# Kernel tuning notes

Hardware: AMD Instinct MI355X
Metric: run time of the kernel (lower is better)

## Reference

```python
import jax, jax.numpy as jnp
import numpy as np

HIDDEN = 2048
N_HEADS = 16
N_KV = 8
HEAD_DIM = 128
EPS = 1e-6
THETA = 1000000.0
T = 2048


def _rmsnorm(x, w):
    # x: [T, h, D]; normalize over last dim
    var = jnp.mean(x * x, axis=-1, keepdims=True)
    return x * jax.lax.rsqrt(var + EPS) * w


def _rope(x, positions):
    # neox-style rotate-half, rotary_dim == head_dim
    D = x.shape[-1]
    inv_freq = 1.0 / (THETA ** (jnp.arange(0, D, 2, dtype=jnp.float32) / D))  # [D/2]
    freqs = positions.astype(jnp.float32)[:, None] * inv_freq  # [T, D/2]
    cos = jnp.cos(freqs)[:, None, :]  # [T, 1, D/2]
    sin = jnp.sin(freqs)[:, None, :]
    x1, x2 = jnp.split(x, 2, axis=-1)
    return jnp.concatenate([x1 * cos - x2 * sin, x2 * cos + x1 * sin], axis=-1)


def setup_inputs() -> dict:
    key = jax.random.key(0)
    ks = jax.random.split(key, 7)
    s = 0.02
    return {
        "positions": jnp.arange(T, dtype=jnp.int32),
        "hidden_states": jax.random.normal(ks[0], (T, HIDDEN), dtype=jnp.float32),
        "wq": jax.random.normal(ks[1], (HIDDEN, N_HEADS * HEAD_DIM), dtype=jnp.float32) * s,
        "wk": jax.random.normal(ks[2], (HIDDEN, N_KV * HEAD_DIM), dtype=jnp.float32) * s,
        "wv": jax.random.normal(ks[3], (HIDDEN, N_KV * HEAD_DIM), dtype=jnp.float32) * s,
        "wo": jax.random.normal(ks[4], (N_HEADS * HEAD_DIM, HIDDEN), dtype=jnp.float32) * s,
        "q_norm_w": jnp.ones((HEAD_DIM,), dtype=jnp.float32),
        "k_norm_w": jnp.ones((HEAD_DIM,), dtype=jnp.float32),
    }


def reference(positions, hidden_states, wq, wk, wv, wo, q_norm_w, k_norm_w):
    q = (hidden_states @ wq).reshape(-1, N_HEADS, HEAD_DIM)
    k = (hidden_states @ wk).reshape(-1, N_KV, HEAD_DIM)
    v = (hidden_states @ wv).reshape(-1, N_KV, HEAD_DIM)
    q = _rmsnorm(q, q_norm_w)
    k = _rmsnorm(k, k_norm_w)
    q = _rope(q, positions)
    k = _rope(k, positions)
    # GQA: expand kv heads
    rep = N_HEADS // N_KV
    k = jnp.repeat(k, rep, axis=1)  # [T, H, D]
    v = jnp.repeat(v, rep, axis=1)
    scale = HEAD_DIM ** -0.5
    scores = jnp.einsum('qhd,khd->hqk', q, k) * scale  # [H, T, T]
    tq = q.shape[0]
    causal = jnp.tril(jnp.ones((tq, tq), dtype=bool))
    scores = jnp.where(causal[None], scores, jnp.finfo(scores.dtype).min)
    probs = jax.nn.softmax(scores, axis=-1)
    o = jnp.einsum('hqk,khd->qhd', probs, v).reshape(tq, N_HEADS * HEAD_DIM)
    return o @ wo
```

## Files before the change

### kernel.cpp

```cpp
#include <hip/hip_runtime.h>
#include <cstdint>

#define TT 2048
#define NH 16
#define NKV 8
#define HD 128
#define SCALE_L2E 0.12751743f
#define SM_M2 16.5f

typedef unsigned short u16;
typedef unsigned int u32;
typedef u16 u16x8 __attribute__((ext_vector_type(8)));
typedef u32 u32x2 __attribute__((ext_vector_type(2)));
typedef __bf16 bf16x8 __attribute__((ext_vector_type(8)));
typedef float f32x4 __attribute__((ext_vector_type(4)));
typedef float f32x16 __attribute__((ext_vector_type(16)));

__device__ inline u16 f2bf(float x){
  u32 u = __builtin_bit_cast(u32, x);
  u = (u + 0x7fffu + ((u >> 16) & 1u)) >> 16;
  return (u16)u;
}
__device__ inline float bf2f(u16 h){
  return __builtin_bit_cast(float, (u32)h << 16);
}
__device__ inline bf16x8 as_bf(u16x8 v){ return __builtin_bit_cast(bf16x8, v); }

__device__ inline void gl_lds16(const void* g, void* l){
  typedef __attribute__((address_space(1))) const void gv_t;
  typedef __attribute__((address_space(3))) void lv_t;
  __builtin_amdgcn_global_load_lds((gv_t*)g, (lv_t*)l, 16, 0, 0);
}

__global__ void cast_f32_bf16(const float* __restrict__ in, u16* __restrict__ out, int n8){
  int i = blockIdx.x * blockDim.x + threadIdx.x;
  if (i < n8){
    const float4* p = (const float4*)(in + (size_t)i * 8);
    float4 a = p[0], b = p[1];
    u16x8 o = { f2bf(a.x), f2bf(a.y), f2bf(a.z), f2bf(a.w),
                f2bf(b.x), f2bf(b.y), f2bf(b.z), f2bf(b.w) };
    *(u16x8*)(out + (size_t)i * 8) = o;
  }
}

__global__ void transpose_cast(const float* __restrict__ in, u16* __restrict__ out, int R, int C){
  __shared__ float tile[64][65];
  int bx = blockIdx.x * 64;
  int by = blockIdx.y * 64;
  int tid = threadIdx.x;
  #pragma unroll
  for (int i = 0; i < 4; ++i){
    int idx = i * 256 + tid;
    int r = idx >> 4, c4 = (idx & 15) * 4;
    float4 v = *(const float4*)&in[(size_t)(by + r) * C + bx + c4];
    tile[r][c4] = v.x; tile[r][c4 + 1] = v.y; tile[r][c4 + 2] = v.z; tile[r][c4 + 3] = v.w;
  }
  __syncthreads();
  #pragma unroll
  for (int i = 0; i < 2; ++i){
    int idx = i * 256 + tid;
    int cc = idx >> 3, s8 = (idx & 7) * 8;
    u16x8 o;
    #pragma unroll
    for (int j = 0; j < 8; ++j) o[j] = f2bf(tile[s8 + j][cc]);
    *(u16x8*)&out[(size_t)(bx + cc) * R + by + s8] = o;
  }
}

template<bool F32OUT>
__global__ __launch_bounds__(512, 2) void gemm8p(const u16* __restrict__ A, const u16* __restrict__ B,
                                                 void* __restrict__ Cv, int Klen,
                                                 int lda, int ldb, int ldc, size_t zstride){
  extern __shared__ u16 smem[];
  const int tid = threadIdx.x;
  const int wv = tid >> 6, ln = tid & 63;
  const int lg = ln >> 4, l15 = ln & 15;
  const int wr = wv >> 2, wc = wv & 3;
  const int nbx = gridDim.x;
  const int orig = blockIdx.x + nbx * blockIdx.y;
  const int cpx = (nbx * gridDim.y) >> 3;
  const int swz = (orig & 7) * cpx + (orig >> 3);
  const int m0 = (swz / nbx) * 128, n0 = (swz % nbx) * 256;
  const int Kofs = blockIdx.z * Klen;
  const u16* Ab0 = A + (size_t)m0 * lda + Kofs;
  const u16* Bb0 = B + (size_t)n0 * ldb + Kofs;
  f32x4 acc[4][4] = {};

  auto stage = [&](int sbuf, int kt, int part){
    u16* base = smem + sbuf * 24576;
    if (part == 0){
      const u16* Ak = Ab0 + kt * 64;
      #pragma unroll
      for (int it = 0; it < 2; ++it){
        int idx = it * 512 + tid;
        int r = idx >> 3, sl = idx & 7, g = sl ^ (r & 7);
        gl_lds16(Ak + (size_t)r * lda + g * 8, base + (it * 512 + wv * 64) * 8);
      }
      const u16* Bk = Bb0 + kt * 64;
      { int idx = tid; int r = idx >> 3, sl = idx & 7, g = sl ^ (r & 7);
        gl_lds16(Bk + (size_t)r * ldb + g * 8, base + (8192 + wv * 64 * 8)); }
    } else {
      const u16* Bk = Bb0 + kt * 64;
      #pragma unroll
      for (int it = 1; it < 4; ++it){
        int idx = it * 512 + tid;
        int r = idx >> 3, sl = idx & 7, g = sl ^ (r & 7);
        gl_lds16(Bk + (size_t)r * ldb + g * 8, base + (8192 + (it * 512 + wv * 64) * 8));
      }
    }
  };

  bf16x8 a0[4], b0[4], a1[4], b1[4];
  auto ldfrags = [&](const u16* lA, bf16x8* af, bf16x8* bf, int kk){
    const u16* lB = lA + 8192;
    #pragma unroll
    for (int mm = 0; mm < 4; mm++){
      int ra = wr * 64 + mm * 16 + l15;
      int sl = (kk * 4 + lg) ^ (ra & 7);
      af[mm] = as_bf(*(const u16x8*)&lA[(ra * 8 + sl) * 8]);
    }
    #pragma unroll
    for (int nn = 0; nn < 4; nn++){
      int cb = wc * 64 + nn * 16 + l15;
      int sl = (kk * 4 + lg) ^ (cb & 7);
      bf[nn] = as_bf(*(const u16x8*)&lB[(cb * 8 + sl) * 8]);
    }
  };
  auto mfma16 = [&](bf16x8* af, bf16x8* bf){
    __builtin_amdgcn_s_setprio(1);
    #pragma unroll
    for (int mm = 0; mm < 4; mm++)
      #pragma unroll
      for (int nn = 0; nn < 4; nn++)
        acc[mm][nn] = __builtin_amdgcn_mfma_f32_16x16x32_bf16(af[mm], bf[nn], acc[mm][nn], 0, 0, 0);
    __builtin_amdgcn_s_setprio(0);
  };

  const int nk = Klen / 64;
  stage(0, 0, 0); stage(0, 0, 1);
  stage(1, 1, 0); stage(1, 1, 1);
  asm volatile("s_waitcnt vmcnt(6)" ::: "memory");
  asm volatile("s_barrier" ::: "memory");
  ldfrags(smem, a0, b0, 0);

  for (int kt = 0; kt < nk; ++kt){
    const u16* lA = smem + (kt % 3) * 24576;
    ldfrags(lA, a1, b1, 1);
    if (kt + 2 < nk) stage((kt + 2) % 3, kt + 2, 0);
    mfma16(a0, b0);
    if (kt + 2 < nk)      asm volatile("s_waitcnt vmcnt(3)" ::: "memory");
    else if (kt + 1 < nk) asm volatile("s_waitcnt vmcnt(0)" ::: "memory");
    asm volatile("s_barrier" ::: "memory");
    if (kt + 1 < nk)
      ldfrags(smem + ((kt + 1) % 3) * 24576, a0, b0, 0);
    if (kt + 2 < nk) stage((kt + 2) % 3, kt + 2, 1);
    mfma16(a1, b1);
    asm volatile("s_barrier" ::: "memory");
  }
  #pragma unroll
  for (int mm = 0; mm < 4; mm++)
    #pragma unroll
    for (int nn = 0; nn < 4; nn++){
      int grow0 = m0 + wr * 64 + mm * 16 + lg * 4;
      int gcol  = n0 + wc * 64 + nn * 16 + l15;
      #pragma unroll
      for (int r = 0; r < 4; r++){
        float v = acc[mm][nn][r];
        if (F32OUT) ((float*)Cv + blockIdx.z * zstride)[(size_t)(grow0 + r) * ldc + gcol] = v;
        else        ((u16*)Cv)[(size_t)(grow0 + r) * ldc + gcol] = f2bf(v);
      }
    }
}

__global__ void add_f32(const float* __restrict__ a, const float* __restrict__ b,
                        float* __restrict__ o, int n4){
  int i = blockIdx.x * blockDim.x + threadIdx.x;
  if (i < n4){
    float4 x = ((const float4*)a)[i], y = ((const float4*)b)[i];
    float4 z = { x.x + y.x, x.y + y.y, x.z + y.z, x.w + y.w };
    ((float4*)o)[i] = z;
  }
}

__global__ void rmsnorm_rope(const u16* __restrict__ QKV, const int* __restrict__ pos,
                             const float* __restrict__ qw, const float* __restrict__ kw,
                             u16* __restrict__ Qr, u16* __restrict__ Kr){
  int gw = (blockIdx.x * blockDim.x + threadIdx.x) >> 6;
  int ln = threadIdx.x & 63;
  int t = gw / 24, idx = gw % 24;
  if (t >= TT) return;
  bool isq = idx < NH;
  int head = isq ? idx : idx - NH;
  const u16* src = QKV + (size_t)t * 4096 + (isq ? head * HD : 2048 + head * HD);
  const float* wgt = isq ? qw : kw;
  float x0 = bf2f(src[ln]), x1 = bf2f(src[ln + 64]);
  float ss = x0 * x0 + x1 * x1;
  #pragma unroll
  for (int off = 32; off; off >>= 1) ss += __shfl_xor(ss, off);
  float r = rsqrtf(ss * (1.0f / 128.0f) + 1e-6f);
  float xn0 = x0 * r * wgt[ln], xn1 = x1 * r * wgt[ln + 64];
  float inv = exp2f(-(float)ln * 0.311430758895690f);
  float ang = (float)pos[t] * inv;
  float c = cosf(ang), s = sinf(ang);
  float o0 = xn0 * c - xn1 * s;
  float o1 = xn1 * c + xn0 * s;
  u16* dst = isq ? (Qr + (size_t)t * 2048 + head * HD) : (Kr + (size_t)t * 1024 + head * HD);
  dst[ln]      = f2bf(o0);
  dst[ln + 64] = f2bf(o1);
}

__global__ void v_transpose(const u16* __restrict__ QKV, u16* __restrict__ Vt){
  __shared__ u16 tile[64][72];
  int kh = blockIdx.z;
  int d0 = blockIdx.y * 64;
  int t0 = blockIdx.x * 64;
  int tid = threadIdx.x;
  #pragma unroll
  for (int it = 0; it < 2; ++it){
    int idx = it * 256 + tid;
    int tr = idx >> 3, seg = idx & 7;
    *(u16x8*)&tile[tr][seg * 8] =
      *(const u16x8*)(QKV + (size_t)(t0 + tr) * 4096 + 3072 + kh * HD + d0 + seg * 8);
  }
  __syncthreads();
  #pragma unroll
  for (int it = 0; it < 2; ++it){
    int idx = it * 256 + tid;
    int dr = idx >> 3, seg = idx & 7;
    u16x8 v;
    #pragma unroll
    for (int j = 0; j < 8; j++) v[j] = tile[seg * 8 + j][dr];
    *(u16x8*)(Vt + ((size_t)kh * HD + d0 + dr) * 2048 + t0 + seg * 8) = v;
  }
}

__global__ __launch_bounds__(512, 4) void attn(const u16* __restrict__ Qr, const u16* __restrict__ Kr,
                                               const u16* __restrict__ Vt, u16* __restrict__ O){
  extern __shared__ u16 smem[];
  u16* Karea = smem;
  u16* Varea = smem + 16384;
  u16* Parea = smem + 32768;
  const int h = blockIdx.y, kh = h >> 1;
  const int qc = (h < 8) ? blockIdx.x : 31 - blockIdx.x;
  const int tid = threadIdx.x, wv = tid >> 6, ln = tid & 63;
  const bool isS = wv < 4;
  const int role = wv & 3;
  const int qw = role & 1, jp = role >> 1;
  const int q5 = ln & 31, hb = ln >> 5;
  const int nit = qc + 1;

  auto stage = [&](int i){
    if (i + 1 < nit){
      u16* Kd = Karea + ((i + 1) & 1) * 8192;
      #pragma unroll
      for (int j = 0; j < 2; ++j){
        int lin = j * 512 + tid;
        int tok = lin >> 4, seg = lin & 15;
        gl_lds16(Kr + (size_t)((i + 1) * 64 + tok) * 1024 + kh * HD + (seg ^ (tok & 7)) * 8,
                 Kd + (j * 512 + wv * 64) * 8);
      }
    }
    if (i < nit){
      u16* Vd = Varea + (i & 1) * 8192;
      #pragma unroll
      for (int j = 0; j < 2; ++j){
        int lin = j * 512 + tid;
        int d = lin >> 3, sl = lin & 7;
        gl_lds16(Vt + (size_t)kh * HD * 2048 + (size_t)d * 2048 + i * 64 + (sl ^ (d & 7)) * 8,
                 Vd + (j * 512 + wv * 64) * 8);
      }
    }
  };

  #pragma unroll
  for (int j = 0; j < 2; ++j){
    int lin = j * 512 + tid;
    int tok = lin >> 4, seg = lin & 15;
    gl_lds16(Kr + (size_t)tok * 1024 + kh * HD + (seg ^ (tok & 7)) * 8,
             Karea + (j * 512 + wv * 64) * 8);
  }

  const u16x8 ones_u = {0x3f80, 0x3f80, 0x3f80, 0x3f80, 0x3f80, 0x3f80, 0x3f80, 0x3f80};
  const bf16x8 onesf = as_bf(ones_u);

  if (isS){
    bf16x8 qf[8];
    {
      const u16* qp = Qr + (size_t)(qc * 64 + qw * 32 + q5) * 2048 + h * HD + hb * 8;
      #pragma unroll
      for (int s = 0; s < 8; ++s) qf[s] = as_bf(*(const u16x8*)(qp + s * 16));
    }
    u16* Pq = Parea + role * 1280 + q5 * 40;
    for (int i = 0; i <= nit; ++i){
      __syncthreads();
      stage(i);
      const int t = 2 * i + jp;
      const int D0 = 32 * t - 64 * qc - 32 * qw;
      const bool act = (i < nit) && (D0 <= 0);
      f32x16 c = {};
      if (act){
        const u16* Kb = Karea + (i & 1) * 8192;
        const int tokIdx = 32 * jp + q5;
        __builtin_amdgcn_s_setprio(1);
        #pragma unroll
        for (int s = 0; s < 8; ++s){
          int seg = (2 * s + hb) ^ (q5 & 7);
          bf16x8 kf = as_bf(*(const u16x8*)&Kb[tokIdx * 128 + seg * 8]);
          c = __builtin_amdgcn_mfma_f32_32x32x16_bf16(kf, qf[s], c, 0, 0, 0);
        }
        __builtin_amdgcn_s_setprio(0);
      }
      asm volatile("s_barrier" ::: "memory");
      if (act){
        const bool diag = (D0 == 0);
        u32 pk[8];
        #pragma unroll
        for (int j = 0; j < 8; ++j){
          float pv[2];
          #pragma unroll
          for (int e = 0; e < 2; ++e){
            int r = 2 * j + e;
            int tok = (r & 3) + 8 * (r >> 2) + 4 * hb;
            float x = c[r] * SCALE_L2E - SM_M2;
            if (diag && tok > q5) x = -1e30f;
            pv[e] = exp2f(x);
          }
          pk[j] = (__builtin_bit_cast(u32, pv[0]) >> 16) |
                  (__builtin_bit_cast(u32, pv[1]) & 0xffff0000u);
        }
        *(u32x2*)&Pq[hb * 4 +  0] = u32x2{pk[0], pk[1]};
        *(u32x2*)&Pq[hb * 4 +  8] = u32x2{pk[2], pk[3]};
        *(u32x2*)&Pq[hb * 4 + 16] = u32x2{pk[4], pk[5]};
        *(u32x2*)&Pq[hb * 4 + 24] = u32x2{pk[6], pk[7]};
      }
    }
    __syncthreads();
    __syncthreads();
  } else {
    f32x16 acc[4] = {};
    f32x16 asum = {};
    const u16* Pw = Parea + role * 1280;
    for (int i = 0; i <= nit; ++i){
      __syncthreads();
      stage(i);
      const int t = 2 * (i - 1) + jp;
      const int D0 = 32 * t - 64 * qc - 32 * qw;
      const bool act = (i >= 1) && (D0 <= 0);
      bf16x8 pf0 = {}, pf1 = {};
      if (act){
        pf0 = as_bf(*(const u16x8*)&Pw[q5 * 40 + hb * 8]);
        pf1 = as_bf(*(const u16x8*)&Pw[q5 * 40 + 16 + hb * 8]);
        asm volatile("s_waitcnt lgkmcnt(0)" ::: "memory");
        __builtin_amdgcn_sched_barrier(0);
      }
      asm volatile("s_barrier" ::: "memory");
      if (act){
        const u16* Vb = Varea + ((i - 1) & 1) * 8192;
        __builtin_amdgcn_s_setprio(1);
        #pragma unroll
        for (int s2 = 0; s2 < 2; ++s2){
          bf16x8 pf = s2 ? pf1 : pf0;
          asum = __builtin_amdgcn_mfma_f32_32x32x16_bf16(pf, onesf, asum, 0, 0, 0);
          #pragma unroll
          for (int dblk = 0; dblk < 4; ++dblk){
            int d = dblk * 32 + q5;
            int sl = (4 * jp + 2 * s2 + hb) ^ (d & 7);
            bf16x8 vf = as_bf(*(const u16x8*)&Vb[d * 64 + sl * 8]);
            acc[dblk] = __builtin_amdgcn_mfma_f32_32x32x16_bf16(pf, vf, acc[dblk], 0, 0, 0);
          }
        }
        __builtin_amdgcn_s_setprio(0);
      }
    }
    __syncthreads();
    float* Ls  = (float*)smem;
    float* LsS = (float*)smem + 8192;
    if (jp == 1){
      #pragma unroll
      for (int dblk = 0; dblk < 4; ++dblk)
        #pragma unroll
        for (int r = 0; r < 16; ++r){
          int qrow = (r & 3) + 8 * (r >> 2) + 4 * hb;
          Ls[qw * 4096 + qrow * 128 + dblk * 32 + q5] = acc[dblk][r];
        }
      if (q5 == 0){
        #pragma unroll
        for (int r = 0; r < 16; ++r){
          int qrow = (r & 3) + 8 * (r >> 2) + 4 * hb;
          LsS[qw * 32 + qrow] = asum[r];
        }
      }
    }
    __syncthreads();
    if (jp == 0){
      #pragma unroll
      for (int r = 0; r < 16; ++r){
        int qrow = (r & 3) + 8 * (r >> 2) + 4 * hb;
        float rs = 1.0f / (asum[r] + LsS[qw * 32 + qrow]);
        int qg = qc * 64 + qw * 32 + qrow;
        #pragma unroll
        for (int dblk = 0; dblk < 4; ++dblk){
          float o = (acc[dblk][r] + Ls[qw * 4096 + qrow * 128 + dblk * 32 + q5]) * rs;
          O[(size_t)qg * 2048 + h * HD + dblk * 32 + q5] = f2bf(o);
        }
      }
    }
  }
}

extern "C" void kernel_launch(void* const* d_in, const int* in_sizes, int n_in,
                              void* d_out, int out_size, void* d_ws, size_t ws_size,
                              hipStream_t stream){
  const int*   positions = (const int*)d_in[0];
  const float* hidden    = (const float*)d_in[1];
  const float* wq        = (const float*)d_in[2];
  const float* wk        = (const float*)d_in[3];
  const float* wv        = (const float*)d_in[4];
  const float* wo        = (const float*)d_in[5];
  const float* qw        = (const float*)d_in[6];
  const float* kw        = (const float*)d_in[7];
  float* out = (float*)d_out;

  char* ws = (char*)d_ws;
  u16* hs   = (u16*)ws; ws += (size_t)2048 * 2048 * 2;
  u16* Wqkv = (u16*)ws; ws += (size_t)4096 * 2048 * 2;
  u16* Wo   = (u16*)ws; ws += (size_t)2048 * 2048 * 2;
  u16* QKV  = (u16*)ws; ws += (size_t)2048 * 4096 * 2;
  u16* Qr   = (u16*)ws; ws += (size_t)2048 * 2048 * 2;
  u16* Kr   = (u16*)ws; ws += (size_t)2048 * 1024 * 2;
  u16* Vt   = (u16*)ws; ws += (size_t)8 * 128 * 2048 * 2;
  u16* O    = (u16*)ws;

  cast_f32_bf16<<<2048, 256, 0, stream>>>(hidden, hs, 2048 * 2048 / 8);
  transpose_cast<<<dim3(32, 32), 256, 0, stream>>>(wq, Wqkv, 2048, 2048);
  transpose_cast<<<dim3(16, 32), 256, 0, stream>>>(wk, Wqkv + (size_t)2048 * 2048, 2048, 1024);
  transpose_cast<<<dim3(16, 32), 256, 0, stream>>>(wv, Wqkv + (size_t)3072 * 2048, 2048, 1024);
  transpose_cast<<<dim3(32, 32), 256, 0, stream>>>(wo, Wo, 2048, 2048);

  gemm8p<false><<<dim3(16, 16, 1), 512, 147456, stream>>>(hs, Wqkv, QKV, 2048, 2048, 2048, 4096, 0);

  rmsnorm_rope<<<2048 * 24 / 4, 256, 0, stream>>>(QKV, positions, qw, kw, Qr, Kr);
  v_transpose<<<dim3(32, 2, 8), 256, 0, stream>>>(QKV, Vt);

  attn<<<dim3(32, 16), 512, 75776, stream>>>(Qr, Kr, Vt, O);

  float* p0 = (float*)QKV;
  gemm8p<true><<<dim3(8, 16, 2), 512, 147456, stream>>>(O, Wo, p0, 1024, 2048, 2048, 2048,
                                                        (size_t)2048 * 2048);
  add_f32<<<4096, 256, 0, stream>>>(p0, p0 + (size_t)2048 * 2048, out, 2048 * 2048 / 4);
}
```

Baseline: 154.3 us.

## Balance causal attention work by pairing query chunks and splitting KV across blocks

Each attention block now handles a pair of query chunks (p and 31-p). The KV range is split between two blocks, so every block walks 16 or 17 key tiles instead of a count that varies with causal position. Partial outputs and row sums for the upper chunk go to fp32 scratch buffers, and a new attn_norm kernel adds and normalizes them. The PV waves now split the head dimension instead of the key dimension, which removes the in-block LDS reduction. This costs an extra kernel launch and fp32 partial traffic, and it reuses the hs/Wqkv workspace as scratch.

```diff
diff --git a/kernel.cpp b/kernel.cpp
--- a/kernel.cpp
+++ b/kernel.cpp
@@ -235,49 +235,60 @@
 }
 
 __global__ __launch_bounds__(512, 4) void attn(const u16* __restrict__ Qr, const u16* __restrict__ Kr,
-                                               const u16* __restrict__ Vt, u16* __restrict__ O){
+                                               const u16* __restrict__ Vt, u16* __restrict__ O,
+                                               float* __restrict__ PB0, float* __restrict__ PB1,
+                                               float* __restrict__ RS0, float* __restrict__ RS1){
   extern __shared__ u16 smem[];
   u16* Karea = smem;
   u16* Varea = smem + 16384;
   u16* Parea = smem + 32768;
+  const int p = blockIdx.x & 15, half = blockIdx.x >> 4;
   const int h = blockIdx.y, kh = h >> 1;
-  const int qc = (h < 8) ? blockIdx.x : 31 - blockIdx.x;
+  const int c1 = p, c2 = 31 - p;
+  const int nst = half ? 16 : 17;
   const int tid = threadIdx.x, wv = tid >> 6, ln = tid & 63;
   const bool isS = wv < 4;
   const int role = wv & 3;
   const int qw = role & 1, jp = role >> 1;
   const int q5 = ln & 31, hb = ln >> 5;
-  const int nit = qc + 1;
-
-  auto stage = [&](int i){
-    if (i + 1 < nit){
-      u16* Kd = Karea + ((i + 1) & 1) * 8192;
-      #pragma unroll
-      for (int j = 0; j < 2; ++j){
-        int lin = j * 512 + tid;
+
+  auto ktof = [&](int j)->int { return half ? (16 - p + j) : ((j <= p) ? j : j - p - 1); };
+  auto chof = [&](int j)->int { return (half == 0 && j <= p) ? c1 : c2; };
+
+  auto stage = [&](int j){
+    if (j + 1 < nst){
+      int kt = ktof(j + 1);
+      u16* Kd = Karea + ((j + 1) & 1) * 8192;
+      #pragma unroll
+      for (int jj = 0; jj < 2; ++jj){
+        int lin = jj * 512 + tid;
         int tok = lin >> 4, seg = lin & 15;
-        gl_lds16(Kr + (size_t)((i + 1) * 64 + tok) * 1024 + kh * HD + (seg ^ (tok & 7)) * 8,
-                 Kd + (j * 512 + wv * 64) * 8);
-      }
-    }
-    if (i < nit){
-      u16* Vd = Varea + (i & 1) * 8192;
-      #pragma unroll
-      for (int j = 0; j < 2; ++j){
-        int lin = j * 512 + tid;
+        gl_lds16(Kr + (size_t)(kt * 64 + tok) * 1024 + kh * HD + (seg ^ (tok & 7)) * 8,
+                 Kd + (jj * 512 + wv * 64) * 8);
+      }
+    }
+    if (j < nst){
+      int kt = ktof(j);
+      u16* Vd = Varea + (j & 1) * 8192;
+      #pragma unroll
+      for (int jj = 0; jj < 2; ++jj){
+        int lin = jj * 512 + tid;
         int d = lin >> 3, sl = lin & 7;
-        gl_lds16(Vt + (size_t)kh * HD * 2048 + (size_t)d * 2048 + i * 64 + (sl ^ (d & 7)) * 8,
-                 Vd + (j * 512 + wv * 64) * 8);
+        gl_lds16(Vt + (size_t)kh * HD * 2048 + (size_t)d * 2048 + kt * 64 + (sl ^ (d & 7)) * 8,
+                 Vd + (jj * 512 + wv * 64) * 8);
       }
     }
   };
 
-  #pragma unroll
-  for (int j = 0; j < 2; ++j){
-    int lin = j * 512 + tid;
-    int tok = lin >> 4, seg = lin & 15;
-    gl_lds16(Kr + (size_t)tok * 1024 + kh * HD + (seg ^ (tok & 7)) * 8,
-             Karea + (j * 512 + wv * 64) * 8);
+  {
+    int kt = ktof(0);
+    #pragma unroll
+    for (int jj = 0; jj < 2; ++jj){
+      int lin = jj * 512 + tid;
+      int tok = lin >> 4, seg = lin & 15;
+      gl_lds16(Kr + (size_t)(kt * 64 + tok) * 1024 + kh * HD + (seg ^ (tok & 7)) * 8,
+               Karea + (jj * 512 + wv * 64) * 8);
+    }
   }
 
   const u16x8 ones_u = {0x3f80, 0x3f80, 0x3f80, 0x3f80, 0x3f80, 0x3f80, 0x3f80, 0x3f80};
@@ -286,47 +297,55 @@
   if (isS){
     bf16x8 qf[8];
     {
-      const u16* qp = Qr + (size_t)(qc * 64 + qw * 32 + q5) * 2048 + h * HD + hb * 8;
+      int c0 = half ? c2 : c1;
+      const u16* qp = Qr + (size_t)(c0 * 64 + qw * 32 + q5) * 2048 + h * HD + hb * 8;
       #pragma unroll
       for (int s = 0; s < 8; ++s) qf[s] = as_bf(*(const u16x8*)(qp + s * 16));
     }
     u16* Pq = Parea + role * 1280 + q5 * 40;
-    for (int i = 0; i <= nit; ++i){
+    for (int j = 0; j <= nst; ++j){
       __syncthreads();
-      stage(i);
-      const int t = 2 * i + jp;
-      const int D0 = 32 * t - 64 * qc - 32 * qw;
-      const bool act = (i < nit) && (D0 <= 0);
+      stage(j);
+      if (half == 0 && j == p + 1){
+        const u16* qp = Qr + (size_t)(c2 * 64 + qw * 32 + q5) * 2048 + h * HD + hb * 8;
+        #pragma unroll
+        for (int s = 0; s < 8; ++s) qf[s] = as_bf(*(const u16x8*)(qp + s * 16));
+      }
+      bool act = false, diag = false;
       f32x16 c = {};
-      if (act){
-        const u16* Kb = Karea + (i & 1) * 8192;
-        const int tokIdx = 32 * jp + q5;
-        __builtin_amdgcn_s_setprio(1);
-        #pragma unroll
-        for (int s = 0; s < 8; ++s){
-          int seg = (2 * s + hb) ^ (q5 & 7);
-          bf16x8 kf = as_bf(*(const u16x8*)&Kb[tokIdx * 128 + seg * 8]);
-          c = __builtin_amdgcn_mfma_f32_32x32x16_bf16(kf, qf[s], c, 0, 0, 0);
+      if (j < nst){
+        int kt = ktof(j), ch = chof(j);
+        int D0 = 32 * (2 * kt + jp) - 64 * ch - 32 * qw;
+        act = (D0 <= 0); diag = (D0 == 0);
+        if (act){
+          const u16* Kb = Karea + (j & 1) * 8192;
+          const int tokIdx = 32 * jp + q5;
+          __builtin_amdgcn_s_setprio(1);
+          #pragma unroll
+          for (int s = 0; s < 8; ++s){
+            int seg = (2 * s + hb) ^ (q5 & 7);
+            bf16x8 kf = as_bf(*(const u16x8*)&Kb[tokIdx * 128 + seg * 8]);
+            c = __builtin_amdgcn_mfma_f32_32x32x16_bf16(kf, qf[s], c, 0, 0, 0);
+          }
+          __builtin_amdgcn_s_setprio(0);
         }
-        __builtin_amdgcn_s_setprio(0);
       }
       asm volatile("s_barrier" ::: "memory");
       if (act){
-        const bool diag = (D0 == 0);
         u32 pk[8];
         #pragma unroll
-        for (int j = 0; j < 8; ++j){
+        for (int jj = 0; jj < 8; ++jj){
           float pv[2];
           #pragma unroll
           for (int e = 0; e < 2; ++e){
-            int r = 2 * j + e;
+            int r = 2 * jj + e;
             int tok = (r & 3) + 8 * (r >> 2) + 4 * hb;
             float x = c[r] * SCALE_L2E - SM_M2;
             if (diag && tok > q5) x = -1e30f;
             pv[e] = exp2f(x);
           }
-          pk[j] = (__builtin_bit_cast(u32, pv[0]) >> 16) |
-                  (__builtin_bit_cast(u32, pv[1]) & 0xffff0000u);
+          pk[jj] = (__builtin_bit_cast(u32, pv[0]) >> 16) |
+                   (__builtin_bit_cast(u32, pv[1]) & 0xffff0000u);
         }
         *(u32x2*)&Pq[hb * 4 +  0] = u32x2{pk[0], pk[1]};
         *(u32x2*)&Pq[hb * 4 +  8] = u32x2{pk[2], pk[3]};
@@ -334,78 +353,104 @@
         *(u32x2*)&Pq[hb * 4 + 24] = u32x2{pk[6], pk[7]};
       }
     }
-    __syncthreads();
-    __syncthreads();
   } else {
-    f32x16 acc[4] = {};
+    f32x16 acc[2] = {};
     f32x16 asum = {};
-    const u16* Pw = Parea + role * 1280;
-    for (int i = 0; i <= nit; ++i){
+    const u16* Pw0 = Parea + (qw + 0) * 1280;
+    const u16* Pw1 = Parea + (qw + 2) * 1280;
+    for (int j = 0; j <= nst; ++j){
       __syncthreads();
-      stage(i);
-      const int t = 2 * (i - 1) + jp;
-      const int D0 = 32 * t - 64 * qc - 32 * qw;
-      const bool act = (i >= 1) && (D0 <= 0);
-      bf16x8 pf0 = {}, pf1 = {};
-      if (act){
-        pf0 = as_bf(*(const u16x8*)&Pw[q5 * 40 + hb * 8]);
-        pf1 = as_bf(*(const u16x8*)&Pw[q5 * 40 + 16 + hb * 8]);
+      stage(j);
+      bool vis0 = false, vis1 = false;
+      int ch = 0;
+      if (j >= 1){
+        int kt = ktof(j - 1); ch = chof(j - 1);
+        vis0 = (32 * (2 * kt + 0) - 64 * ch - 32 * qw) <= 0;
+        vis1 = (32 * (2 * kt + 1) - 64 * ch - 32 * qw) <= 0;
+      }
+      bf16x8 pf0 = {}, pf1 = {}, pf2 = {}, pf3 = {};
+      if (vis0){
+        pf0 = as_bf(*(const u16x8*)&Pw0[q5 * 40 + hb * 8]);
+        pf1 = as_bf(*(const u16x8*)&Pw0[q5 * 40 + 16 + hb * 8]);
+        if (vis1){
+          pf2 = as_bf(*(const u16x8*)&Pw1[q5 * 40 + hb * 8]);
+          pf3 = as_bf(*(const u16x8*)&Pw1[q5 * 40 + 16 + hb * 8]);
+        }
         asm volatile("s_waitcnt lgkmcnt(0)" ::: "memory");
         __builtin_amdgcn_sched_barrier(0);
       }
       asm volatile("s_barrier" ::: "memory");
-      if (act){
-        const u16* Vb = Varea + ((i - 1) & 1) * 8192;
+      if (vis0){
+        const u16* Vb = Varea + ((j - 1) & 1) * 8192;
         __builtin_amdgcn_s_setprio(1);
+        asum = __builtin_amdgcn_mfma_f32_32x32x16_bf16(pf0, onesf, asum, 0, 0, 0);
+        asum = __builtin_amdgcn_mfma_f32_32x32x16_bf16(pf1, onesf, asum, 0, 0, 0);
         #pragma unroll
-        for (int s2 = 0; s2 < 2; ++s2){
-          bf16x8 pf = s2 ? pf1 : pf0;
-          asum = __builtin_amdgcn_mfma_f32_32x32x16_bf16(pf, onesf, asum, 0, 0, 0);
+        for (int db = 0; db < 2; ++db){
+          int d = (jp * 2 + db) * 32 + q5;
+          bf16x8 v0 = as_bf(*(const u16x8*)&Vb[d * 64 + ((0 + hb) ^ (d & 7)) * 8]);
+          bf16x8 v1 = as_bf(*(const u16x8*)&Vb[d * 64 + ((2 + hb) ^ (d & 7)) * 8]);
+          acc[db] = __builtin_amdgcn_mfma_f32_32x32x16_bf16(pf0, v0, acc[db], 0, 0, 0);
+          acc[db] = __builtin_amdgcn_mfma_f32_32x32x16_bf16(pf1, v1, acc[db], 0, 0, 0);
+        }
+        if (vis1){
+          asum = __builtin_amdgcn_mfma_f32_32x32x16_bf16(pf2, onesf, asum, 0, 0, 0);
+          asum = __builtin_amdgcn_mfma_f32_32x32x16_bf16(pf3, onesf, asum, 0, 0, 0);
           #pragma unroll
-          for (int dblk = 0; dblk < 4; ++dblk){
-            int d = dblk * 32 + q5;
-            int sl = (4 * jp + 2 * s2 + hb) ^ (d & 7);
-            bf16x8 vf = as_bf(*(const u16x8*)&Vb[d * 64 + sl * 8]);
-            acc[dblk] = __builtin_amdgcn_mfma_f32_32x32x16_bf16(pf, vf, acc[dblk], 0, 0, 0);
+          for (int db = 0; db < 2; ++db){
+            int d = (jp * 2 + db) * 32 + q5;
+            bf16x8 v2 = as_bf(*(const u16x8*)&Vb[d * 64 + ((4 + hb) ^ (d & 7)) * 8]);
+            bf16x8 v3 = as_bf(*(const u16x8*)&Vb[d * 64 + ((6 + hb) ^ (d & 7)) * 8]);
+            acc[db] = __builtin_amdgcn_mfma_f32_32x32x16_bf16(pf2, v2, acc[db], 0, 0, 0);
+            acc[db] = __builtin_amdgcn_mfma_f32_32x32x16_bf16(pf3, v3, acc[db], 0, 0, 0);
           }
         }
         __builtin_amdgcn_s_setprio(0);
       }
-    }
-    __syncthreads();
-    float* Ls  = (float*)smem;
-    float* LsS = (float*)smem + 8192;
-    if (jp == 1){
-      #pragma unroll
-      for (int dblk = 0; dblk < 4; ++dblk)
+      if (half == 0 && j == p + 1){
         #pragma unroll
         for (int r = 0; r < 16; ++r){
           int qrow = (r & 3) + 8 * (r >> 2) + 4 * hb;
-          Ls[qw * 4096 + qrow * 128 + dblk * 32 + q5] = acc[dblk][r];
+          float rinv = 1.0f / asum[r];
+          int qg = c1 * 64 + qw * 32 + qrow;
+          #pragma unroll
+          for (int db = 0; db < 2; ++db)
+            O[(size_t)qg * 2048 + h * HD + (jp * 2 + db) * 32 + q5] = f2bf(acc[db][r] * rinv);
         }
-      if (q5 == 0){
-        #pragma unroll
-        for (int r = 0; r < 16; ++r){
-          int qrow = (r & 3) + 8 * (r >> 2) + 4 * hb;
-          LsS[qw * 32 + qrow] = asum[r];
-        }
-      }
-    }
-    __syncthreads();
-    if (jp == 0){
-      #pragma unroll
-      for (int r = 0; r < 16; ++r){
-        int qrow = (r & 3) + 8 * (r >> 2) + 4 * hb;
-        float rs = 1.0f / (asum[r] + LsS[qw * 32 + qrow]);
-        int qg = qc * 64 + qw * 32 + qrow;
-        #pragma unroll
-        for (int dblk = 0; dblk < 4; ++dblk){
-          float o = (acc[dblk][r] + Ls[qw * 4096 + qrow * 128 + dblk * 32 + q5]) * rs;
-          O[(size_t)qg * 2048 + h * HD + dblk * 32 + q5] = f2bf(o);
-        }
-      }
-    }
-  }
+        acc[0] = f32x16{}; acc[1] = f32x16{}; asum = f32x16{};
+      }
+    }
+    float* PB = half ? PB1 : PB0;
+    float* RS = half ? RS1 : RS0;
+    #pragma unroll
+    for (int r = 0; r < 16; ++r){
+      int qrow = (r & 3) + 8 * (r >> 2) + 4 * hb;
+      int qg = c2 * 64 + qw * 32 + qrow;
+      size_t rb = (size_t)(qg - 1024) * 2048 + h * HD;
+      #pragma unroll
+      for (int db = 0; db < 2; ++db)
+        PB[rb + (jp * 2 + db) * 32 + q5] = acc[db][r];
+      if (jp == 0 && q5 == 0) RS[(qg - 1024) * 16 + h] = asum[r];
+    }
+  }
+}
+
+__global__ void attn_norm(const float* __restrict__ PB0, const float* __restrict__ PB1,
+                          const float* __restrict__ RS0, const float* __restrict__ RS1,
+                          u16* __restrict__ O){
+  int idx = blockIdx.x * blockDim.x + threadIdx.x;
+  int rp = idx >> 8;
+  int col = (idx & 255) * 8;
+  int h = col >> 7;
+  float rinv = 1.0f / (RS0[rp * 16 + h] + RS1[rp * 16 + h]);
+  size_t base = (size_t)rp * 2048 + col;
+  float4 a0 = *(const float4*)&PB0[base],     a1 = *(const float4*)&PB0[base + 4];
+  float4 b0 = *(const float4*)&PB1[base],     b1 = *(const float4*)&PB1[base + 4];
+  u16x8 o = { f2bf((a0.x + b0.x) * rinv), f2bf((a0.y + b0.y) * rinv),
+              f2bf((a0.z + b0.z) * rinv), f2bf((a0.w + b0.w) * rinv),
+              f2bf((a1.x + b1.x) * rinv), f2bf((a1.y + b1.y) * rinv),
+              f2bf((a1.z + b1.z) * rinv), f2bf((a1.w + b1.w) * rinv) };
+  *(u16x8*)&O[(size_t)(1024 + rp) * 2048 + col] = o;
 }
 
 extern "C" void kernel_launch(void* const* d_in, const int* in_sizes, int n_in,
@@ -431,6 +476,11 @@
   u16* Vt   = (u16*)ws; ws += (size_t)8 * 128 * 2048 * 2;
   u16* O    = (u16*)ws;
 
+  float* PB0 = (float*)hs;
+  float* PB1 = (float*)Wqkv;
+  float* RS0 = (float*)(Wqkv + (size_t)4194304);
+  float* RS1 = RS0 + 16384;
+
   cast_f32_bf16<<<2048, 256, 0, stream>>>(hidden, hs, 2048 * 2048 / 8);
   transpose_cast<<<dim3(32, 32), 256, 0, stream>>>(wq, Wqkv, 2048, 2048);
   transpose_cast<<<dim3(16, 32), 256, 0, stream>>>(wk, Wqkv + (size_t)2048 * 2048, 2048, 1024);
@@ -442,7 +492,8 @@
   rmsnorm_rope<<<2048 * 24 / 4, 256, 0, stream>>>(QKV, positions, qw, kw, Qr, Kr);
   v_transpose<<<dim3(32, 2, 8), 256, 0, stream>>>(QKV, Vt);
 
-  attn<<<dim3(32, 16), 512, 75776, stream>>>(Qr, Kr, Vt, O);
+  attn<<<dim3(32, 16), 512, 75776, stream>>>(Qr, Kr, Vt, O, PB0, PB1, RS0, RS1);
+  attn_norm<<<1024, 256, 0, stream>>>(PB0, PB1, RS0, RS1, O);
 
   float* p0 = (float*)QKV;
   gemm8p<true><<<dim3(8, 16, 2), 512, 147456, stream>>>(O, Wo, p0, 1024, 2048, 2048, 2048,
```

Measured after the change: 161.0 us. 4.3% more time.

## Double-buffer P tile in attention to drop the mid-iteration barrier

Applied to the files above, without the earlier changes.

Gives the softmax-probability (P) staging area in LDS two buffers indexed by iteration parity. The score waves can then write iteration i while the PV waves read iteration i-1, which removes the extra s_barrier and lgkmcnt wait inside each loop iteration. It also splits the QK^T MFMA accumulation into two independent chains summed afterward, XOR-swizzles the P layout to cut bank conflicts, and flattens the PV loop. LDS use per block grows to 81920 bytes, which still allows two blocks per CU if the CU has 160KB of LDS.

```diff
diff --git a/kernel.cpp b/kernel.cpp
--- a/kernel.cpp
+++ b/kernel.cpp
@@ -248,6 +248,7 @@
   const int qw = role & 1, jp = role >> 1;
   const int q5 = ln & 31, hb = ln >> 5;
   const int nit = qc + 1;
+  const int xr = (q5 & 3) << 1;
 
   auto stage = [&](int i){
     if (i + 1 < nit){
@@ -290,28 +291,31 @@
       #pragma unroll
       for (int s = 0; s < 8; ++s) qf[s] = as_bf(*(const u16x8*)(qp + s * 16));
     }
-    u16* Pq = Parea + role * 1280 + q5 * 40;
     for (int i = 0; i <= nit; ++i){
       __syncthreads();
       stage(i);
       const int t = 2 * i + jp;
       const int D0 = 32 * t - 64 * qc - 32 * qw;
       const bool act = (i < nit) && (D0 <= 0);
-      f32x16 c = {};
       if (act){
         const u16* Kb = Karea + (i & 1) * 8192;
         const int tokIdx = 32 * jp + q5;
+        f32x16 ca = {}, cb = {};
         __builtin_amdgcn_s_setprio(1);
         #pragma unroll
-        for (int s = 0; s < 8; ++s){
+        for (int s = 0; s < 4; ++s){
           int seg = (2 * s + hb) ^ (q5 & 7);
           bf16x8 kf = as_bf(*(const u16x8*)&Kb[tokIdx * 128 + seg * 8]);
-          c = __builtin_amdgcn_mfma_f32_32x32x16_bf16(kf, qf[s], c, 0, 0, 0);
+          ca = __builtin_amdgcn_mfma_f32_32x32x16_bf16(kf, qf[s], ca, 0, 0, 0);
+        }
+        #pragma unroll
+        for (int s = 4; s < 8; ++s){
+          int seg = (2 * s + hb) ^ (q5 & 7);
+          bf16x8 kf = as_bf(*(const u16x8*)&Kb[tokIdx * 128 + seg * 8]);
+          cb = __builtin_amdgcn_mfma_f32_32x32x16_bf16(kf, qf[s], cb, 0, 0, 0);
         }
         __builtin_amdgcn_s_setprio(0);
-      }
-      asm volatile("s_barrier" ::: "memory");
-      if (act){
+        f32x16 c = ca + cb;
         const bool diag = (D0 == 0);
         u32 pk[8];
         #pragma unroll
@@ -328,10 +332,11 @@
           pk[j] = (__builtin_bit_cast(u32, pv[0]) >> 16) |
                   (__builtin_bit_cast(u32, pv[1]) & 0xffff0000u);
         }
-        *(u32x2*)&Pq[hb * 4 +  0] = u32x2{pk[0], pk[1]};
-        *(u32x2*)&Pq[hb * 4 +  8] = u32x2{pk[2], pk[3]};
-        *(u32x2*)&Pq[hb * 4 + 16] = u32x2{pk[4], pk[5]};
-        *(u32x2*)&Pq[hb * 4 + 24] = u32x2{pk[6], pk[7]};
+        u16* Pq = Parea + (i & 1) * 4096 + role * 1024 + q5 * 32;
+        *(u32x2*)&Pq[((hb + 0) ^ xr) * 4] = u32x2{pk[0], pk[1]};
+        *(u32x2*)&Pq[((hb + 2) ^ xr) * 4] = u32x2{pk[2], pk[3]};
+        *(u32x2*)&Pq[((hb + 4) ^ xr) * 4] = u32x2{pk[4], pk[5]};
+        *(u32x2*)&Pq[((hb + 6) ^ xr) * 4] = u32x2{pk[6], pk[7]};
       }
     }
     __syncthreads();
@@ -339,35 +344,27 @@
   } else {
     f32x16 acc[4] = {};
     f32x16 asum = {};
-    const u16* Pw = Parea + role * 1280;
     for (int i = 0; i <= nit; ++i){
       __syncthreads();
       stage(i);
       const int t = 2 * (i - 1) + jp;
       const int D0 = 32 * t - 64 * qc - 32 * qw;
       const bool act = (i >= 1) && (D0 <= 0);
-      bf16x8 pf0 = {}, pf1 = {};
       if (act){
-        pf0 = as_bf(*(const u16x8*)&Pw[q5 * 40 + hb * 8]);
-        pf1 = as_bf(*(const u16x8*)&Pw[q5 * 40 + 16 + hb * 8]);
-        asm volatile("s_waitcnt lgkmcnt(0)" ::: "memory");
-        __builtin_amdgcn_sched_barrier(0);
-      }
-      asm volatile("s_barrier" ::: "memory");
-      if (act){
+        const u16* Pq = Parea + ((i - 1) & 1) * 4096 + role * 1024 + q5 * 32;
+        bf16x8 pf0 = as_bf(*(const u16x8*)&Pq[((2 * hb + 0) ^ xr) * 4]);
+        bf16x8 pf1 = as_bf(*(const u16x8*)&Pq[((2 * hb + 4) ^ xr) * 4]);
         const u16* Vb = Varea + ((i - 1) & 1) * 8192;
         __builtin_amdgcn_s_setprio(1);
-        #pragma unroll
-        for (int s2 = 0; s2 < 2; ++s2){
-          bf16x8 pf = s2 ? pf1 : pf0;
-          asum = __builtin_amdgcn_mfma_f32_32x32x16_bf16(pf, onesf, asum, 0, 0, 0);
-          #pragma unroll
-          for (int dblk = 0; dblk < 4; ++dblk){
-            int d = dblk * 32 + q5;
-            int sl = (4 * jp + 2 * s2 + hb) ^ (d & 7);
-            bf16x8 vf = as_bf(*(const u16x8*)&Vb[d * 64 + sl * 8]);
-            acc[dblk] = __builtin_amdgcn_mfma_f32_32x32x16_bf16(pf, vf, acc[dblk], 0, 0, 0);
-          }
+        asum = __builtin_amdgcn_mfma_f32_32x32x16_bf16(pf0, onesf, asum, 0, 0, 0);
+        asum = __builtin_amdgcn_mfma_f32_32x32x16_bf16(pf1, onesf, asum, 0, 0, 0);
+        #pragma unroll
+        for (int dblk = 0; dblk < 4; ++dblk){
+          int d = dblk * 32 + q5;
+          bf16x8 v0 = as_bf(*(const u16x8*)&Vb[d * 64 + ((4 * jp + 0 + hb) ^ (d & 7)) * 8]);
+          bf16x8 v1 = as_bf(*(const u16x8*)&Vb[d * 64 + ((4 * jp + 2 + hb) ^ (d & 7)) * 8]);
+          acc[dblk] = __builtin_amdgcn_mfma_f32_32x32x16_bf16(pf0, v0, acc[dblk], 0, 0, 0);
+          acc[dblk] = __builtin_amdgcn_mfma_f32_32x32x16_bf16(pf1, v1, acc[dblk], 0, 0, 0);
         }
         __builtin_amdgcn_s_setprio(0);
       }
@@ -442,7 +439,7 @@
   rmsnorm_rope<<<2048 * 24 / 4, 256, 0, stream>>>(QKV, positions, qw, kw, Qr, Kr);
   v_transpose<<<dim3(32, 2, 8), 256, 0, stream>>>(QKV, Vt);
 
-  attn<<<dim3(32, 16), 512, 75776, stream>>>(Qr, Kr, Vt, O);
+  attn<<<dim3(32, 16), 512, 81920, stream>>>(Qr, Kr, Vt, O);
 
   float* p0 = (float*)QKV;
   gemm8p<true><<<dim3(8, 16, 2), 512, 147456, stream>>>(O, Wo, p0, 1024, 2048, 2048, 2048,
```

New measurement: 154.2 us. No clear change (-0.0%).
